# Kernel optimization log

Hardware: AMD Instinct MI355X
Metric: run time of the kernel (lower is better)

Reference implementation:

```python
import jax, jax.numpy as jnp
import numpy as np


def gcn_conv(x, W, b, src, dst, n):
    """PyG GCNConv: D^-1/2 (A+I) D^-1/2 X W + b, with added self-loops."""
    xw = x @ W  # [N, out]
    loop = jnp.arange(n, dtype=src.dtype)
    s = jnp.concatenate([src, loop])
    d = jnp.concatenate([dst, loop])
    deg = jax.ops.segment_sum(jnp.ones_like(d, dtype=xw.dtype), d, num_segments=n)
    dinv = jax.lax.rsqrt(jnp.maximum(deg, 1.0))
    norm = dinv[s] * dinv[d]  # [E+N]
    msg = xw[s] * norm[:, None]  # [E+N, out]
    return jax.ops.segment_sum(msg, d, num_segments=n) + b


def mean_pool(h, batch, num_graphs):
    s = jax.ops.segment_sum(h, batch, num_segments=num_graphs)
    cnt = jax.ops.segment_sum(jnp.ones((h.shape[0],), h.dtype), batch, num_segments=num_graphs)
    return s / jnp.maximum(cnt, 1.0)[:, None]


def setup_inputs() -> dict:
    key = jax.random.key(0)
    ks = jax.random.split(key, 12)
    N, E, F_dim, H_dim, K = 50000, 1600000, 128, 128, 32
    G = 64
    X = jax.random.normal(ks[0], (N, F_dim), dtype=jnp.float32)
    ei_feat = jax.random.randint(ks[1], (2, E), 0, N, dtype=jnp.int64)
    batch = jnp.sort(jax.random.randint(ks[2], (N,), 0, G, dtype=jnp.int64))
    sc = 1.0 / np.sqrt(H_dim)
    W1 = jax.random.normal(ks[3], (F_dim, H_dim), dtype=jnp.float32) * sc
    b1 = jnp.zeros((H_dim,), jnp.float32)
    W2 = jax.random.normal(ks[4], (H_dim, K), dtype=jnp.float32) * sc
    b2 = jnp.zeros((K,), jnp.float32)
    mW1 = jax.random.normal(ks[5], (H_dim, H_dim), dtype=jnp.float32) * sc
    mb1 = jnp.zeros((H_dim,), jnp.float32)
    mW2 = jax.random.normal(ks[6], (K, K), dtype=jnp.float32) * (1.0 / np.sqrt(K))
    mb2 = jnp.zeros((K,), jnp.float32)
    return {"X": X, "W1": W1, "b1": b1, "W2": W2, "b2": b2,
            "mW1": mW1, "mb1": mb1, "mW2": mW2, "mb2": mb2,
            "ei_feat": ei_feat, "batch": batch, "num_graphs": G}


def reference(X, W1, b1, W2, b2, mW1, mb1, mW2, mb2, ei_feat, batch, num_graphs):
    N = X.shape[0]
    src, dst = ei_feat[0], ei_feat[1]
    h = jax.nn.elu(gcn_conv(X, W1, b1, src, dst, N))  # [N, H]
    master_h = mean_pool(h, batch, num_graphs)  # [G, H]
    h = h + jax.nn.relu(master_h @ mW1 + mb1)[batch]
    Z = gcn_conv(h, W2, b2, src, dst, N)  # [N, K]
    master_z = mean_pool(Z, batch, num_graphs)  # [G, K]
    Z = Z + jax.nn.relu(master_z @ mW2 + mb2)[batch]
    return jax.nn.softmax(Z, axis=1)
```

## Files before the change

### kernel.cpp

```cpp
#include <hip/hip_runtime.h>
#include <hip/hip_bf16.h>
#include <hip/hip_fp16.h>

#define DEV_INLINE __device__ __forceinline__

static DEV_INLINE float4 ld4(const float* p){ return *reinterpret_cast<const float4*>(p); }

#define GNUM 64
#define CHUNK 4096
#define MAXNB 1024

__global__ __launch_bounds__(256) void k_hist(const int* __restrict__ dst, int E, int NB,
                                              int* __restrict__ bcnt){
    __shared__ int cnt[MAXNB];
    int t = threadIdx.x; int base0 = blockIdx.x*CHUNK;
    for (int i=t;i<NB;i+=256) cnt[i]=0;
    __syncthreads();
    int tot = E - base0; if (tot > CHUNK) tot = CHUNK;
    #pragma unroll
    for (int k=0;k<16;k++){
        int o = t + k*256;
        if (o < tot) atomicAdd(&cnt[dst[base0+o]>>7], 1);
    }
    __syncthreads();
    for (int i=t;i<NB;i+=256) if (cnt[i]) atomicAdd(&bcnt[i], cnt[i]);
}

__global__ void k_scan1b(const int* __restrict__ in, int* __restrict__ out, int M, int total,
                         const int* __restrict__ batch, int N, int* __restrict__ gstart){
    __shared__ int ws[4];
    int t = threadIdx.x;
    int i0 = t*4;
    int c0=(i0+0<M)?in[i0+0]:0, c1=(i0+1<M)?in[i0+1]:0;
    int c2=(i0+2<M)?in[i0+2]:0, c3=(i0+3<M)?in[i0+3]:0;
    int tsum=c0+c1+c2+c3;
    int lane=t&63, w=t>>6;
    int x=tsum;
    for (int off=1;off<64;off<<=1){ int yv=__shfl_up(x,off); if (lane>=off) x+=yv; }
    if (lane==63) ws[w]=x;
    __syncthreads();
    if (t==0){ int a=0; for (int i=0;i<4;i++){ int tmp=ws[i]; ws[i]=a; a+=tmp; } }
    __syncthreads();
    int ex = x - tsum + ws[w];
    if (i0+0<M) out[i0+0]=ex; ex+=c0;
    if (i0+1<M) out[i0+1]=ex; ex+=c1;
    if (i0+2<M) out[i0+2]=ex; ex+=c2;
    if (i0+3<M) out[i0+3]=ex;
    if (t==0 && total>=0) out[M]=total;
    if (t <= GNUM){
        int lo = 0, hi = N;
        while (lo < hi){ int mid = (lo+hi)>>1; if (batch[mid] < t) lo = mid+1; else hi = mid; }
        gstart[t] = lo;
    }
}

__global__ __launch_bounds__(256) void k_scatter(const int* __restrict__ src, const int* __restrict__ dst,
                                                 int E, int NB, const int* __restrict__ bbase,
                                                 int* __restrict__ bfill, unsigned* __restrict__ ebuf){
    __shared__ int cnt[MAXNB];
    __shared__ int pfx[MAXNB];
    __shared__ int gbase[MAXNB];
    __shared__ unsigned stage[CHUNK];
    __shared__ int ws[4];
    int t = threadIdx.x; int base0 = blockIdx.x*CHUNK;
    int tot = E - base0; if (tot > CHUNK) tot = CHUNK;
    for (int i=t;i<NB;i+=256) cnt[i]=0;
    __syncthreads();
    unsigned v[16]; int rk[16];
    #pragma unroll
    for (int k=0;k<16;k++){
        int o = t + k*256;
        if (o < tot){
            int e = base0 + o;
            int s = src[e], d = dst[e];
            v[k] = (unsigned)s | ((unsigned)d<<16);
            rk[k] = atomicAdd(&cnt[d>>7], 1);
        } else { v[k]=0u; rk[k]=-1; }
    }
    __syncthreads();
    int i0 = t*4;
    int c0=(i0+0<NB)?cnt[i0+0]:0, c1=(i0+1<NB)?cnt[i0+1]:0;
    int c2=(i0+2<NB)?cnt[i0+2]:0, c3=(i0+3<NB)?cnt[i0+3]:0;
    int tsum=c0+c1+c2+c3;
    int lane=t&63, w=t>>6;
    int x=tsum;
    for (int off=1;off<64;off<<=1){ int yv=__shfl_up(x,off); if (lane>=off) x+=yv; }
    if (lane==63) ws[w]=x;
    __syncthreads();
    if (t==0){ int a=0; for (int i=0;i<4;i++){ int tmp=ws[i]; ws[i]=a; a+=tmp; } }
    __syncthreads();
    int ex = x - tsum + ws[w];
    if (i0+0<NB) pfx[i0+0]=ex; ex+=c0;
    if (i0+1<NB) pfx[i0+1]=ex; ex+=c1;
    if (i0+2<NB) pfx[i0+2]=ex; ex+=c2;
    if (i0+3<NB) pfx[i0+3]=ex;
    __syncthreads();
    for (int i=t;i<NB;i+=256){
        int c = cnt[i];
        gbase[i] = c ? (bbase[i] + atomicAdd(&bfill[i], c)) : 0;
    }
    __syncthreads();
    #pragma unroll
    for (int k=0;k<16;k++) if (rk[k]>=0){ int b = (int)(v[k]>>23); stage[pfx[b]+rk[k]] = v[k]; }
    __syncthreads();
    for (int j=t;j<tot;j+=256){
        unsigned u = stage[j];
        int b = (int)(u>>23);
        ebuf[gbase[b] + (j - pfx[b])] = u;
    }
}

__global__ __launch_bounds__(256) void k_bucket_finish(const unsigned* __restrict__ ebuf,
                                                       const int* __restrict__ bbase,
                                                       int* __restrict__ rs, int* __restrict__ csr,
                                                       float* __restrict__ dinv, int N, int E){
    __shared__ int c2[128];
    __shared__ int rsl[128];
    __shared__ int ws[4];
    int b = blockIdx.x, t = threadIdx.x;
    if (t < 128) c2[t] = 0;
    __syncthreads();
    int s0 = bbase[b], s1 = bbase[b+1];
    for (int j = s0+t; j < s1; j += 256)
        atomicAdd(&c2[(ebuf[j]>>16)&127], 1);
    __syncthreads();
    int v = (t < 128) ? c2[t] : 0;
    int lane = t & 63, w = t >> 6;
    int x = v;
    for (int off=1; off<64; off<<=1){
        int yv = __shfl_up(x, off);
        if (lane >= off) x += yv;
    }
    if (lane == 63) ws[w] = x;
    __syncthreads();
    if (t < 128){
        int ex = x - v + ((w == 1) ? ws[0] : 0);
        rsl[t] = s0 + ex;
        int node = (b<<7) + t;
        if (node < N){
            rs[node] = s0 + ex;
            dinv[node] = rsqrtf((float)(v + 1));
        }
    }
    if (b == (int)gridDim.x - 1 && t == 0) rs[N] = E;
    __syncthreads();
    if (t < 128) c2[t] = 0;
    __syncthreads();
    for (int j = s0+t; j < s1; j += 256){
        unsigned u = ebuf[j];
        int ld = (u>>16)&127;
        int p = atomicAdd(&c2[ld], 1);
        csr[rsl[ld]+p] = (int)(u & 0xffffu);
    }
}

__global__ __launch_bounds__(256) void k_gemm1(const float* __restrict__ X, const float* __restrict__ W1,
                                               const float* __restrict__ dinv, __half* __restrict__ yh, int N){
    __shared__ float Ws[128*128];
    __shared__ float Xs[32*128];
    int t = threadIdx.x;
    int row0 = blockIdx.x * 32;
    if (blockIdx.x==0 && t < 32)
        reinterpret_cast<uint2*>(yh + (size_t)N*128)[t] = make_uint2(0u,0u);
    {
        const float4* Wg = (const float4*)W1;
        float4* Wl = (float4*)Ws;
        #pragma unroll
        for (int i=0;i<16;i++) Wl[t + i*256] = Wg[t + i*256];
    }
    {
        float4* Xl = (float4*)Xs;
        const float4* Xg = (const float4*)X;
        #pragma unroll
        for (int i=0;i<4;i++){
            int fi = t + i*256;
            int r = fi >> 5;
            float4 v = make_float4(0.f,0.f,0.f,0.f);
            if (row0 + r < N) v = Xg[(size_t)(row0+r)*32 + (fi & 31)];
            Xl[fi] = v;
        }
    }
    __syncthreads();
    int tc = t & 31, tr = t >> 5;
    float4 acc0={0,0,0,0}, acc1={0,0,0,0}, acc2={0,0,0,0}, acc3={0,0,0,0};
    for (int k=0;k<128;k+=4){
        float4 w0 = ld4(&Ws[(k+0)*128 + tc*4]);
        float4 w1 = ld4(&Ws[(k+1)*128 + tc*4]);
        float4 w2 = ld4(&Ws[(k+2)*128 + tc*4]);
        float4 w3 = ld4(&Ws[(k+3)*128 + tc*4]);
        #define ROWSTEP(ACC, RR) { float4 xr = ld4(&Xs[(4*tr+(RR))*128 + k]); \
            ACC.x += xr.x*w0.x + xr.y*w1.x + xr.z*w2.x + xr.w*w3.x; \
            ACC.y += xr.x*w0.y + xr.y*w1.y + xr.z*w2.y + xr.w*w3.y; \
            ACC.z += xr.x*w0.z + xr.y*w1.z + xr.z*w2.z + xr.w*w3.z; \
            ACC.w += xr.x*w0.w + xr.y*w1.w + xr.z*w2.w + xr.w*w3.w; }
        ROWSTEP(acc0,0) ROWSTEP(acc1,1) ROWSTEP(acc2,2) ROWSTEP(acc3,3)
        #undef ROWSTEP
    }
    #define STORESTEP(ACC, RR) { int row = row0 + 4*tr + (RR); if (row < N){ \
        float dv = dinv[row]; \
        __half2 p0 = __floats2half2_rn(ACC.x*dv, ACC.y*dv); \
        __half2 p1 = __floats2half2_rn(ACC.z*dv, ACC.w*dv); \
        uint2 stv; stv.x = *(unsigned*)&p0; stv.y = *(unsigned*)&p1; \
        *reinterpret_cast<uint2*>(&yh[(size_t)row*128 + tc*4]) = stv; } }
    STORESTEP(acc0,0) STORESTEP(acc1,1) STORESTEP(acc2,2) STORESTEP(acc3,3)
    #undef STORESTEP
}

__global__ void k_agg1(const __half* __restrict__ yh, const float* __restrict__ dinv,
                       const float* __restrict__ b1, const int* __restrict__ rs,
                       const int* __restrict__ csr, __half* __restrict__ h, int N){
    int wid = (int)((blockIdx.x * blockDim.x + threadIdx.x) >> 6);
    if (wid >= N) return;
    int lane = threadIdx.x & 63;
    int half = lane >> 5, hl = lane & 31;
    int beg = rs[wid], end = rs[wid+1];
    int len = end - beg;
    int len0 = (len + 1) >> 1;
    int hbeg = beg + (half ? len0 : 0);
    int hlen = half ? (len - len0) : len0;
    const __half* ybase = yh + hl*4;
    float4 acc = make_float4(0.f,0.f,0.f,0.f);
    if (half == 0){
        uint2 u = *reinterpret_cast<const uint2*>(ybase + (size_t)wid*128);
        float2 f0 = __half22float2(*(__half2*)&u.x), f1 = __half22float2(*(__half2*)&u.y);
        acc.x=f0.x; acc.y=f0.y; acc.z=f1.x; acc.w=f1.y;
    }
    int iters = (len0 + 31) >> 5;
    for (int c=0;c<iters;c++){
        int o = c*32 + hl;
        int idx = (o < hlen) ? csr[hbeg + o] : N;
        int tmax = len0 - c*32; if (tmax > 32) tmax = 32;
        int nch = (tmax + 3) >> 2;
        __half2 a0 = __float2half2_rn(0.f), a1 = __float2half2_rn(0.f);
        for (int ch=0; ch<nch; ++ch){
            int tb = (half<<5) + ch*4;
            int s0 = __shfl(idx, tb+0);
            int s1 = __shfl(idx, tb+1);
            int s2 = __shfl(idx, tb+2);
            int s3 = __shfl(idx, tb+3);
            uint2 u0 = *reinterpret_cast<const uint2*>(ybase + (size_t)s0*128);
            uint2 u1 = *reinterpret_cast<const uint2*>(ybase + (size_t)s1*128);
            uint2 u2 = *reinterpret_cast<const uint2*>(ybase + (size_t)s2*128);
            uint2 u3 = *reinterpret_cast<const uint2*>(ybase + (size_t)s3*128);
            a0 = __hadd2(a0, *(__half2*)&u0.x); a1 = __hadd2(a1, *(__half2*)&u0.y);
            a0 = __hadd2(a0, *(__half2*)&u1.x); a1 = __hadd2(a1, *(__half2*)&u1.y);
            a0 = __hadd2(a0, *(__half2*)&u2.x); a1 = __hadd2(a1, *(__half2*)&u2.y);
            a0 = __hadd2(a0, *(__half2*)&u3.x); a1 = __hadd2(a1, *(__half2*)&u3.y);
        }
        float2 f0 = __half22float2(a0), f1 = __half22float2(a1);
        acc.x += f0.x; acc.y += f0.y; acc.z += f1.x; acc.w += f1.y;
    }
    acc.x += __shfl_xor(acc.x, 32);
    acc.y += __shfl_xor(acc.y, 32);
    acc.z += __shfl_xor(acc.z, 32);
    acc.w += __shfl_xor(acc.w, 32);
    if (half == 0){
        float dv = dinv[wid];
        float4 bb = ld4(&b1[hl*4]);
        float4 o;
        o.x = dv*acc.x + bb.x; o.y = dv*acc.y + bb.y;
        o.z = dv*acc.z + bb.z; o.w = dv*acc.w + bb.w;
        o.x = o.x > 0.f ? o.x : expm1f(o.x);
        o.y = o.y > 0.f ? o.y : expm1f(o.y);
        o.z = o.z > 0.f ? o.z : expm1f(o.z);
        o.w = o.w > 0.f ? o.w : expm1f(o.w);
        __half2 p0 = __floats2half2_rn(o.x, o.y);
        __half2 p1 = __floats2half2_rn(o.z, o.w);
        uint2 stv; stv.x = *(unsigned*)&p0; stv.y = *(unsigned*)&p1;
        *reinterpret_cast<uint2*>(&h[(size_t)wid*128 + hl*4]) = stv;
    }
}

__global__ void k_mpoolh(const __half* __restrict__ hsrc, const int* __restrict__ gstart,
                         float* __restrict__ msum){
    int g = blockIdx.x, part = blockIdx.y, P = gridDim.y;
    int c = threadIdx.x;
    int s0 = gstart[g], s1 = gstart[g+1];
    int len = s1 - s0;
    int per = (len + P - 1) / P;
    int rbeg = s0 + part*per, rend = rbeg + per; if (rend > s1) rend = s1;
    float sx = 0.f, sy = 0.f;
    const __half2* h2 = (const __half2*)hsrc;
    for (int r = rbeg; r < rend; ++r){
        float2 f = __half22float2(h2[(size_t)r*64 + c]);
        sx += f.x; sy += f.y;
    }
    if (rend > rbeg){
        atomicAdd(&msum[g*128 + 2*c], sx);
        atomicAdd(&msum[g*128 + 2*c+1], sy);
    }
}

__global__ void k_mpool(const float* __restrict__ srcm, const int* __restrict__ gstart,
                        float* __restrict__ msum, int C){
    int g = blockIdx.x, part = blockIdx.y, P = gridDim.y;
    int c = threadIdx.x;
    if (c >= C) return;
    int s0 = gstart[g], s1 = gstart[g+1];
    int len = s1 - s0;
    int per = (len + P - 1) / P;
    int rbeg = s0 + part*per, rend = rbeg + per; if (rend > s1) rend = s1;
    float sum = 0.f;
    for (int r = rbeg; r < rend; ++r) sum += srcm[(size_t)r*C + c];
    if (rend > rbeg) atomicAdd(&msum[g*C + c], sum);
}

__global__ void k_mlp1(const float* __restrict__ msum, const int* __restrict__ gstart,
                       const float* __restrict__ mW1, const float* __restrict__ mb1,
                       float* __restrict__ r1){
    int g = blockIdx.x, c = threadIdx.x;
    int cnt = gstart[g+1] - gstart[g];
    float inv = 1.f / (float)(cnt > 1 ? cnt : 1);
    float acc = mb1[c];
    for (int k=0;k<128;k++) acc = fmaf(msum[g*128+k]*inv, mW1[k*128+c], acc);
    r1[g*128+c] = fmaxf(acc, 0.f);
}

__global__ void k_mlp2(const float* __restrict__ msum2, const int* __restrict__ gstart,
                       const float* __restrict__ mW2, const float* __restrict__ mb2,
                       float* __restrict__ r2){
    int g = blockIdx.x, c = threadIdx.x;
    if (c >= 32) return;
    int cnt = gstart[g+1] - gstart[g];
    float inv = 1.f / (float)(cnt > 1 ? cnt : 1);
    float acc = mb2[c];
    for (int k=0;k<32;k++) acc = fmaf(msum2[g*32+k]*inv, mW2[k*32+c], acc);
    r2[g*32+c] = fmaxf(acc, 0.f);
}

__global__ __launch_bounds__(256) void k_gemm2(const __half* __restrict__ h, const float* __restrict__ vn,
                                               const int* __restrict__ batch, const float* __restrict__ W2,
                                               const float* __restrict__ dinv, __half* __restrict__ y2, int N){
    __shared__ float W2s[128*32];
    int t = threadIdx.x;
    if (blockIdx.x==0 && t < 8)
        reinterpret_cast<uint2*>(y2 + (size_t)N*32)[t] = make_uint2(0u,0u);
    {
        float4* Wl = (float4*)W2s;
        const float4* Wg = (const float4*)W2;
        #pragma unroll
        for (int i=0;i<4;i++) Wl[t + i*256] = Wg[t + i*256];
    }
    __syncthreads();
    int row0 = blockIdx.x*64;
    int tc = t & 7, trg = t >> 3;
    int ra = row0 + 2*trg, rb = ra + 1;
    bool oka = ra < N, okb = rb < N;
    const __half* hpa = h + (size_t)(oka ? ra : 0)*128;
    const __half* hpb = h + (size_t)(okb ? rb : 0)*128;
    const float* vpa = vn + (size_t)(oka ? batch[ra] : 0)*128;
    const float* vpb = vn + (size_t)(okb ? batch[rb] : 0)*128;
    float4 acca={0,0,0,0}, accb={0,0,0,0};
    for (int k=0;k<128;k+=4){
        float4 w0 = ld4(&W2s[(k+0)*32 + tc*4]);
        float4 w1 = ld4(&W2s[(k+1)*32 + tc*4]);
        float4 w2 = ld4(&W2s[(k+2)*32 + tc*4]);
        float4 w3 = ld4(&W2s[(k+3)*32 + tc*4]);
        {
            uint2 u = *reinterpret_cast<const uint2*>(&hpa[k]);
            float2 f0 = __half22float2(*(__half2*)&u.x), f1 = __half22float2(*(__half2*)&u.y);
            float4 bb = ld4(vpa + k);
            float ax=f0.x+bb.x, ay=f0.y+bb.y, az=f1.x+bb.z, aw=f1.y+bb.w;
            acca.x += ax*w0.x + ay*w1.x + az*w2.x + aw*w3.x;
            acca.y += ax*w0.y + ay*w1.y + az*w2.y + aw*w3.y;
            acca.z += ax*w0.z + ay*w1.z + az*w2.z + aw*w3.z;
            acca.w += ax*w0.w + ay*w1.w + az*w2.w + aw*w3.w;
        }
        {
            uint2 u = *reinterpret_cast<const uint2*>(&hpb[k]);
            float2 f0 = __half22float2(*(__half2*)&u.x), f1 = __half22float2(*(__half2*)&u.y);
            float4 bb = ld4(vpb + k);
            float ax=f0.x+bb.x, ay=f0.y+bb.y, az=f1.x+bb.z, aw=f1.y+bb.w;
            accb.x += ax*w0.x + ay*w1.x + az*w2.x + aw*w3.x;
            accb.y += ax*w0.y + ay*w1.y + az*w2.y + aw*w3.y;
            accb.z += ax*w0.z + ay*w1.z + az*w2.z + aw*w3.z;
            accb.w += ax*w0.w + ay*w1.w + az*w2.w + aw*w3.w;
        }
    }
    if (oka){
        float dv = dinv[ra];
        __half2 p0 = __floats2half2_rn(acca.x*dv, acca.y*dv);
        __half2 p1 = __floats2half2_rn(acca.z*dv, acca.w*dv);
        uint2 stv; stv.x = *(unsigned*)&p0; stv.y = *(unsigned*)&p1;
        *reinterpret_cast<uint2*>(&y2[(size_t)ra*32 + tc*4]) = stv;
    }
    if (okb){
        float dv = dinv[rb];
        __half2 p0 = __floats2half2_rn(accb.x*dv, accb.y*dv);
        __half2 p1 = __floats2half2_rn(accb.z*dv, accb.w*dv);
        uint2 stv; stv.x = *(unsigned*)&p0; stv.y = *(unsigned*)&p1;
        *reinterpret_cast<uint2*>(&y2[(size_t)rb*32 + tc*4]) = stv;
    }
}

__global__ void k_agg2h(const __half* __restrict__ y2, const float* __restrict__ dinv,
                        const float* __restrict__ b2, const int* __restrict__ rs,
                        const int* __restrict__ csr, float* __restrict__ Z, int N){
    int wid = (int)((blockIdx.x*blockDim.x + threadIdx.x) >> 6);
    if (wid >= N) return;
    int lane = threadIdx.x & 63;
    int q = lane >> 4, ql = lane & 15;
    int beg = rs[wid], end = rs[wid+1], len = end-beg;
    int qlen = (len + 3) >> 2;
    int qbeg = beg + q*qlen;
    int qend = qbeg + qlen; if (qend > end) qend = end;
    int mylen = qend - qbeg; if (mylen < 0) mylen = 0;
    const __half2* ybase = (const __half2*)(y2) + ql;
    float sx = 0.f, sy = 0.f;
    int iters = (qlen + 15) >> 4;
    for (int c=0;c<iters;c++){
        int o = c*16 + ql;
        int idx = (o < mylen) ? csr[qbeg + o] : N;
        int tmax = qlen - c*16; if (tmax > 16) tmax = 16;
        int nch = (tmax + 3) >> 2;
        __half2 a = __float2half2_rn(0.f);
        for (int ch=0; ch<nch; ++ch){
            int tb = (q<<4) + ch*4;
            int s0 = __shfl(idx, tb+0);
            int s1 = __shfl(idx, tb+1);
            int s2 = __shfl(idx, tb+2);
            int s3 = __shfl(idx, tb+3);
            __half2 v0 = ybase[(size_t)s0*16];
            __half2 v1 = ybase[(size_t)s1*16];
            __half2 v2 = ybase[(size_t)s2*16];
            __half2 v3 = ybase[(size_t)s3*16];
            a = __hadd2(a, v0); a = __hadd2(a, v1);
            a = __hadd2(a, v2); a = __hadd2(a, v3);
        }
        float2 f = __half22float2(a);
        sx += f.x; sy += f.y;
    }
    sx += __shfl_xor(sx, 16); sy += __shfl_xor(sy, 16);
    sx += __shfl_xor(sx, 32); sy += __shfl_xor(sy, 32);
    if (q==0){
        float2 self = __half22float2(ybase[(size_t)wid*16]);
        sx += self.x; sy += self.y;
        float dv = dinv[wid];
        float2 o;
        o.x = dv*sx + b2[ql*2];
        o.y = dv*sy + b2[ql*2+1];
        *reinterpret_cast<float2*>(&Z[(size_t)wid*32 + ql*2]) = o;
    }
}

__global__ void k_softmax(float* __restrict__ Z, const float* __restrict__ r2,
                          const int* __restrict__ batch, int N){
    int r = blockIdx.x*8 + (threadIdx.x>>5);
    int c = threadIdx.x & 31;
    if (r >= N) return;
    float z = Z[(size_t)r*32+c] + r2[batch[r]*32 + c];
    float m = z;
    #pragma unroll
    for (int off=16; off>=1; off>>=1) m = fmaxf(m, __shfl_xor(m, off));
    float e = expf(z - m);
    float s = e;
    #pragma unroll
    for (int off=16; off>=1; off>>=1) s += __shfl_xor(s, off);
    Z[(size_t)r*32+c] = e / s;
}

extern "C" void kernel_launch(void* const* d_in, const int* in_sizes, int n_in,
                              void* d_out, int out_size, void* d_ws, size_t ws_size,
                              hipStream_t stream){
    const float* X   = (const float*)d_in[0];
    const float* W1  = (const float*)d_in[1];
    const float* b1  = (const float*)d_in[2];
    const float* W2  = (const float*)d_in[3];
    const float* b2  = (const float*)d_in[4];
    const float* mW1 = (const float*)d_in[5];
    const float* mb1 = (const float*)d_in[6];
    const float* mW2 = (const float*)d_in[7];
    const float* mb2 = (const float*)d_in[8];
    const int*   ei  = (const int*)d_in[9];
    const int*   batch = (const int*)d_in[10];
    int N = in_sizes[0] / 128;
    int E = in_sizes[9] / 2;
    const int* src = ei;
    const int* dst = ei + E;
    float* Zout = (float*)d_out;

    char* wsp = (char*)d_ws;
    size_t off = 0;
    auto alloc = [&](size_t bytes)->char*{
        char* p = wsp + off; off += (bytes + 255) & ~(size_t)255; return p;
    };
    int*   bcnt  = (int*)  alloc((size_t)MAXNB*4);
    int*   bfill = (int*)  alloc((size_t)MAXNB*4);
    float* msum  = (float*)alloc((size_t)GNUM*128*4);
    float* msum2 = (float*)alloc((size_t)GNUM*32*4);
    size_t zero_bytes = off;
    int*   bbase = (int*)  alloc((size_t)(MAXNB+1)*4);
    int*   rs    = (int*)  alloc((size_t)(N+1)*4);
    int*   gstart= (int*)  alloc((GNUM+1)*4);
    unsigned* ebuf = (unsigned*)alloc((size_t)E*4);
    int*   csr   = (int*)  alloc((size_t)E*4);
    float* dinvp = (float*)alloc((size_t)N*4);
    __half* yh   = (__half*)alloc((size_t)(N+1)*128*2);
    __half* h    = (__half*)alloc((size_t)N*128*2);
    __half* y2h  = (__half*)alloc((size_t)(N+1)*32*2);
    float* r1buf = (float*)alloc((size_t)GNUM*128*4);
    float* r2buf = (float*)alloc((size_t)GNUM*32*4);
    (void)ws_size; (void)n_in; (void)out_size;

    hipMemsetAsync(d_ws, 0, zero_bytes, stream);

    int NB = (N + 127) >> 7;
    int EB = (E + CHUNK-1) / CHUNK;

    k_hist         <<<EB, 256, 0, stream>>>(dst, E, NB, bcnt);
    k_scan1b       <<<1, 256, 0, stream>>>(bcnt, bbase, NB, E, batch, N, gstart);
    k_scatter      <<<EB, 256, 0, stream>>>(src, dst, E, NB, bbase, bfill, ebuf);
    k_bucket_finish<<<NB, 256, 0, stream>>>(ebuf, bbase, rs, csr, dinvp, N, E);

    k_gemm1 <<<(N+31)/32, 256, 0, stream>>>(X, W1, dinvp, yh, N);
    k_agg1  <<<(N+3)/4, 256, 0, stream>>>(yh, dinvp, b1, rs, csr, h, N);

    k_mpoolh<<<dim3(GNUM,8), 64, 0, stream>>>(h, gstart, msum);
    k_mlp1  <<<GNUM, 128, 0, stream>>>(msum, gstart, mW1, mb1, r1buf);

    k_gemm2 <<<(N+63)/64, 256, 0, stream>>>(h, r1buf, batch, W2, dinvp, y2h, N);
    k_agg2h <<<(N+3)/4, 256, 0, stream>>>(y2h, dinvp, b2, rs, csr, Zout, N);

    k_mpool <<<dim3(GNUM,8), 64, 0, stream>>>(Zout, gstart, msum2, 32);
    k_mlp2  <<<GNUM, 64, 0, stream>>>(msum2, gstart, mW2, mb2, r2buf);
    k_softmax<<<(N+7)/8, 256, 0, stream>>>(Zout, r2buf, batch, N);
}
```

Before: 259.7 us.

## Use MFMA fp16 for first GEMM, 16-bit CSR indices, wider gather loads

The first GEMM now runs on MFMA 16x16x32 fp16 instructions, reading W1 from a transposed, padded fp16 copy built by a new prep kernel, and converting X to fp16 in registers. CSR column indices shrink from 32-bit to 16-bit to cut index traffic. Both aggregation kernels switch to wider vector gathers (uint4 in layer 1, uint2 in layer 2) with more edge splits per wave. The aim is lower GEMM compute cost and less memory traffic in the gathers. Casting X to fp16 adds rounding error, and 16-bit indices rely on the node id fitting in 16 bits, which the existing bucket encoding already assumes.

Result: faster. 241.3 us (-7.1%).

```diff
diff --git a/kernel.cpp b/kernel.cpp
--- a/kernel.cpp
+++ b/kernel.cpp
@@ -9,6 +9,9 @@
 #define GNUM 64
 #define CHUNK 4096
 #define MAXNB 1024
+
+typedef _Float16 half8 __attribute__((ext_vector_type(8)));
+typedef float floatx4 __attribute__((ext_vector_type(4)));
 
 __global__ __launch_bounds__(256) void k_hist(const int* __restrict__ dst, int E, int NB,
                                               int* __restrict__ bcnt){
@@ -112,7 +115,7 @@
 
 __global__ __launch_bounds__(256) void k_bucket_finish(const unsigned* __restrict__ ebuf,
                                                        const int* __restrict__ bbase,
-                                                       int* __restrict__ rs, int* __restrict__ csr,
+                                                       int* __restrict__ rs, unsigned short* __restrict__ csr,
                                                        float* __restrict__ dinv, int N, int E){
     __shared__ int c2[128];
     __shared__ int rsl[128];
@@ -150,124 +153,132 @@
         unsigned u = ebuf[j];
         int ld = (u>>16)&127;
         int p = atomicAdd(&c2[ld], 1);
-        csr[rsl[ld]+p] = (int)(u & 0xffffu);
-    }
-}
-
-__global__ __launch_bounds__(256) void k_gemm1(const float* __restrict__ X, const float* __restrict__ W1,
+        csr[rsl[ld]+p] = (unsigned short)(u & 0xffffu);
+    }
+}
+
+__global__ void k_prep(const float* __restrict__ W1, __half* __restrict__ w1t){
+    int f = blockIdx.x*256 + threadIdx.x;
+    int c = f >> 7, k = f & 127;
+    w1t[c*136 + k] = __float2half(W1[k*128 + c]);
+}
+
+__global__ __launch_bounds__(256) void k_gemm1(const float* __restrict__ X, const __half* __restrict__ w1t,
                                                const float* __restrict__ dinv, __half* __restrict__ yh, int N){
-    __shared__ float Ws[128*128];
-    __shared__ float Xs[32*128];
+    __shared__ __half Wl[128*136];
     int t = threadIdx.x;
-    int row0 = blockIdx.x * 32;
     if (blockIdx.x==0 && t < 32)
         reinterpret_cast<uint2*>(yh + (size_t)N*128)[t] = make_uint2(0u,0u);
     {
-        const float4* Wg = (const float4*)W1;
-        float4* Wl = (float4*)Ws;
+        const uint4* g = (const uint4*)w1t;
+        uint4* l = (uint4*)Wl;
+        for (int i = t; i < 2176; i += 256) l[i] = g[i];
+    }
+    __syncthreads();
+    int wv = t>>6, lane = t&63;
+    int r0 = blockIdx.x*64 + wv*16;
+    if (r0 >= N) return;
+    int lr = lane & 15, lg = lane >> 4;
+    int r = r0 + lr;
+    bool rok = r < N;
+    const float* xrow = X + (size_t)(rok ? r : 0)*128;
+    floatx4 acc[8];
+    #pragma unroll
+    for (int i=0;i<8;i++) acc[i] = (floatx4){0.f,0.f,0.f,0.f};
+    #pragma unroll
+    for (int ks=0; ks<4; ks++){
+        int k0 = ks*32 + lg*8;
+        float4 xa = ld4(xrow + k0);
+        float4 xb = ld4(xrow + k0 + 4);
+        half8 bfrag;
+        bfrag[0]=(_Float16)xa.x; bfrag[1]=(_Float16)xa.y; bfrag[2]=(_Float16)xa.z; bfrag[3]=(_Float16)xa.w;
+        bfrag[4]=(_Float16)xb.x; bfrag[5]=(_Float16)xb.y; bfrag[6]=(_Float16)xb.z; bfrag[7]=(_Float16)xb.w;
         #pragma unroll
-        for (int i=0;i<16;i++) Wl[t + i*256] = Wg[t + i*256];
-    }
-    {
-        float4* Xl = (float4*)Xs;
-        const float4* Xg = (const float4*)X;
+        for (int ct=0; ct<8; ct++){
+            half8 afrag = *reinterpret_cast<const half8*>(&Wl[(ct*16 + lr)*136 + k0]);
+            acc[ct] = __builtin_amdgcn_mfma_f32_16x16x32_f16(afrag, bfrag, acc[ct], 0, 0, 0);
+        }
+    }
+    if (rok){
+        float dv = dinv[r];
         #pragma unroll
-        for (int i=0;i<4;i++){
-            int fi = t + i*256;
-            int r = fi >> 5;
-            float4 v = make_float4(0.f,0.f,0.f,0.f);
-            if (row0 + r < N) v = Xg[(size_t)(row0+r)*32 + (fi & 31)];
-            Xl[fi] = v;
-        }
-    }
-    __syncthreads();
-    int tc = t & 31, tr = t >> 5;
-    float4 acc0={0,0,0,0}, acc1={0,0,0,0}, acc2={0,0,0,0}, acc3={0,0,0,0};
-    for (int k=0;k<128;k+=4){
-        float4 w0 = ld4(&Ws[(k+0)*128 + tc*4]);
-        float4 w1 = ld4(&Ws[(k+1)*128 + tc*4]);
-        float4 w2 = ld4(&Ws[(k+2)*128 + tc*4]);
-        float4 w3 = ld4(&Ws[(k+3)*128 + tc*4]);
-        #define ROWSTEP(ACC, RR) { float4 xr = ld4(&Xs[(4*tr+(RR))*128 + k]); \
-            ACC.x += xr.x*w0.x + xr.y*w1.x + xr.z*w2.x + xr.w*w3.x; \
-            ACC.y += xr.x*w0.y + xr.y*w1.y + xr.z*w2.y + xr.w*w3.y; \
-            ACC.z += xr.x*w0.z + xr.y*w1.z + xr.z*w2.z + xr.w*w3.z; \
-            ACC.w += xr.x*w0.w + xr.y*w1.w + xr.z*w2.w + xr.w*w3.w; }
-        ROWSTEP(acc0,0) ROWSTEP(acc1,1) ROWSTEP(acc2,2) ROWSTEP(acc3,3)
-        #undef ROWSTEP
-    }
-    #define STORESTEP(ACC, RR) { int row = row0 + 4*tr + (RR); if (row < N){ \
-        float dv = dinv[row]; \
-        __half2 p0 = __floats2half2_rn(ACC.x*dv, ACC.y*dv); \
-        __half2 p1 = __floats2half2_rn(ACC.z*dv, ACC.w*dv); \
-        uint2 stv; stv.x = *(unsigned*)&p0; stv.y = *(unsigned*)&p1; \
-        *reinterpret_cast<uint2*>(&yh[(size_t)row*128 + tc*4]) = stv; } }
-    STORESTEP(acc0,0) STORESTEP(acc1,1) STORESTEP(acc2,2) STORESTEP(acc3,3)
-    #undef STORESTEP
+        for (int ct=0; ct<8; ct++){
+            __half2 p0 = __floats2half2_rn(acc[ct][0]*dv, acc[ct][1]*dv);
+            __half2 p1 = __floats2half2_rn(acc[ct][2]*dv, acc[ct][3]*dv);
+            uint2 stv; stv.x = *(unsigned*)&p0; stv.y = *(unsigned*)&p1;
+            *reinterpret_cast<uint2*>(&yh[(size_t)r*128 + ct*16 + lg*4]) = stv;
+        }
+    }
 }
 
 __global__ void k_agg1(const __half* __restrict__ yh, const float* __restrict__ dinv,
                        const float* __restrict__ b1, const int* __restrict__ rs,
-                       const int* __restrict__ csr, __half* __restrict__ h, int N){
+                       const unsigned short* __restrict__ csr, __half* __restrict__ h, int N){
     int wid = (int)((blockIdx.x * blockDim.x + threadIdx.x) >> 6);
     if (wid >= N) return;
     int lane = threadIdx.x & 63;
-    int half = lane >> 5, hl = lane & 31;
+    int q = lane >> 4, ql = lane & 15;
     int beg = rs[wid], end = rs[wid+1];
     int len = end - beg;
-    int len0 = (len + 1) >> 1;
-    int hbeg = beg + (half ? len0 : 0);
-    int hlen = half ? (len - len0) : len0;
-    const __half* ybase = yh + hl*4;
-    float4 acc = make_float4(0.f,0.f,0.f,0.f);
-    if (half == 0){
-        uint2 u = *reinterpret_cast<const uint2*>(ybase + (size_t)wid*128);
-        float2 f0 = __half22float2(*(__half2*)&u.x), f1 = __half22float2(*(__half2*)&u.y);
-        acc.x=f0.x; acc.y=f0.y; acc.z=f1.x; acc.w=f1.y;
-    }
-    int iters = (len0 + 31) >> 5;
+    int qlen = (len + 3) >> 2;
+    int qbeg = beg + q*qlen;
+    int qend = qbeg + qlen; if (qend > end) qend = end;
+    int mylen = qend - qbeg; if (mylen < 0) mylen = 0;
+    const uint4* base = reinterpret_cast<const uint4*>(yh) + ql;
+    float f0=0.f,f1=0.f,f2=0.f,f3=0.f,f4=0.f,f5=0.f,f6=0.f,f7=0.f;
+    int iters = (qlen + 15) >> 4;
     for (int c=0;c<iters;c++){
-        int o = c*32 + hl;
-        int idx = (o < hlen) ? csr[hbeg + o] : N;
-        int tmax = len0 - c*32; if (tmax > 32) tmax = 32;
+        int o = c*16 + ql;
+        int idx = (o < mylen) ? (int)csr[qbeg + o] : N;
+        int tmax = qlen - c*16; if (tmax > 16) tmax = 16;
         int nch = (tmax + 3) >> 2;
-        __half2 a0 = __float2half2_rn(0.f), a1 = __float2half2_rn(0.f);
+        __half2 a0 = __float2half2_rn(0.f), a1 = a0, a2 = a0, a3 = a0;
         for (int ch=0; ch<nch; ++ch){
-            int tb = (half<<5) + ch*4;
+            int tb = (q<<4) + ch*4;
             int s0 = __shfl(idx, tb+0);
             int s1 = __shfl(idx, tb+1);
             int s2 = __shfl(idx, tb+2);
             int s3 = __shfl(idx, tb+3);
-            uint2 u0 = *reinterpret_cast<const uint2*>(ybase + (size_t)s0*128);
-            uint2 u1 = *reinterpret_cast<const uint2*>(ybase + (size_t)s1*128);
-            uint2 u2 = *reinterpret_cast<const uint2*>(ybase + (size_t)s2*128);
-            uint2 u3 = *reinterpret_cast<const uint2*>(ybase + (size_t)s3*128);
+            uint4 u0 = base[(size_t)s0*16];
+            uint4 u1 = base[(size_t)s1*16];
+            uint4 u2 = base[(size_t)s2*16];
+            uint4 u3 = base[(size_t)s3*16];
             a0 = __hadd2(a0, *(__half2*)&u0.x); a1 = __hadd2(a1, *(__half2*)&u0.y);
+            a2 = __hadd2(a2, *(__half2*)&u0.z); a3 = __hadd2(a3, *(__half2*)&u0.w);
             a0 = __hadd2(a0, *(__half2*)&u1.x); a1 = __hadd2(a1, *(__half2*)&u1.y);
+            a2 = __hadd2(a2, *(__half2*)&u1.z); a3 = __hadd2(a3, *(__half2*)&u1.w);
             a0 = __hadd2(a0, *(__half2*)&u2.x); a1 = __hadd2(a1, *(__half2*)&u2.y);
+            a2 = __hadd2(a2, *(__half2*)&u2.z); a3 = __hadd2(a3, *(__half2*)&u2.w);
             a0 = __hadd2(a0, *(__half2*)&u3.x); a1 = __hadd2(a1, *(__half2*)&u3.y);
-        }
-        float2 f0 = __half22float2(a0), f1 = __half22float2(a1);
-        acc.x += f0.x; acc.y += f0.y; acc.z += f1.x; acc.w += f1.y;
-    }
-    acc.x += __shfl_xor(acc.x, 32);
-    acc.y += __shfl_xor(acc.y, 32);
-    acc.z += __shfl_xor(acc.z, 32);
-    acc.w += __shfl_xor(acc.w, 32);
-    if (half == 0){
+            a2 = __hadd2(a2, *(__half2*)&u3.z); a3 = __hadd2(a3, *(__half2*)&u3.w);
+        }
+        float2 t0 = __half22float2(a0); f0 += t0.x; f1 += t0.y;
+        float2 t1 = __half22float2(a1); f2 += t1.x; f3 += t1.y;
+        float2 t2 = __half22float2(a2); f4 += t2.x; f5 += t2.y;
+        float2 t3 = __half22float2(a3); f6 += t3.x; f7 += t3.y;
+    }
+    f0 += __shfl_xor(f0,16); f1 += __shfl_xor(f1,16); f2 += __shfl_xor(f2,16); f3 += __shfl_xor(f3,16);
+    f4 += __shfl_xor(f4,16); f5 += __shfl_xor(f5,16); f6 += __shfl_xor(f6,16); f7 += __shfl_xor(f7,16);
+    f0 += __shfl_xor(f0,32); f1 += __shfl_xor(f1,32); f2 += __shfl_xor(f2,32); f3 += __shfl_xor(f3,32);
+    f4 += __shfl_xor(f4,32); f5 += __shfl_xor(f5,32); f6 += __shfl_xor(f6,32); f7 += __shfl_xor(f7,32);
+    if (q == 0){
+        uint4 su = base[(size_t)wid*16];
+        float2 s0 = __half22float2(*(__half2*)&su.x); f0 += s0.x; f1 += s0.y;
+        float2 s1 = __half22float2(*(__half2*)&su.y); f2 += s1.x; f3 += s1.y;
+        float2 s2 = __half22float2(*(__half2*)&su.z); f4 += s2.x; f5 += s2.y;
+        float2 s3 = __half22float2(*(__half2*)&su.w); f6 += s3.x; f7 += s3.y;
         float dv = dinv[wid];
-        float4 bb = ld4(&b1[hl*4]);
-        float4 o;
-        o.x = dv*acc.x + bb.x; o.y = dv*acc.y + bb.y;
-        o.z = dv*acc.z + bb.z; o.w = dv*acc.w + bb.w;
-        o.x = o.x > 0.f ? o.x : expm1f(o.x);
-        o.y = o.y > 0.f ? o.y : expm1f(o.y);
-        o.z = o.z > 0.f ? o.z : expm1f(o.z);
-        o.w = o.w > 0.f ? o.w : expm1f(o.w);
-        __half2 p0 = __floats2half2_rn(o.x, o.y);
-        __half2 p1 = __floats2half2_rn(o.z, o.w);
-        uint2 stv; stv.x = *(unsigned*)&p0; stv.y = *(unsigned*)&p1;
-        *reinterpret_cast<uint2*>(&h[(size_t)wid*128 + hl*4]) = stv;
+        float4 ba = ld4(&b1[ql*8]), bb = ld4(&b1[ql*8+4]);
+        float o0 = dv*f0+ba.x, o1 = dv*f1+ba.y, o2 = dv*f2+ba.z, o3 = dv*f3+ba.w;
+        float o4 = dv*f4+bb.x, o5 = dv*f5+bb.y, o6 = dv*f6+bb.z, o7 = dv*f7+bb.w;
+        o0 = o0>0.f?o0:expm1f(o0); o1 = o1>0.f?o1:expm1f(o1);
+        o2 = o2>0.f?o2:expm1f(o2); o3 = o3>0.f?o3:expm1f(o3);
+        o4 = o4>0.f?o4:expm1f(o4); o5 = o5>0.f?o5:expm1f(o5);
+        o6 = o6>0.f?o6:expm1f(o6); o7 = o7>0.f?o7:expm1f(o7);
+        __half2 p0 = __floats2half2_rn(o0,o1), p1 = __floats2half2_rn(o2,o3);
+        __half2 p2 = __floats2half2_rn(o4,o5), p3 = __floats2half2_rn(o6,o7);
+        uint4 stv; stv.x=*(unsigned*)&p0; stv.y=*(unsigned*)&p1; stv.z=*(unsigned*)&p2; stv.w=*(unsigned*)&p3;
+        *reinterpret_cast<uint4*>(&h[(size_t)wid*128 + ql*8]) = stv;
     }
 }
 
@@ -395,51 +406,56 @@
 
 __global__ void k_agg2h(const __half* __restrict__ y2, const float* __restrict__ dinv,
                         const float* __restrict__ b2, const int* __restrict__ rs,
-                        const int* __restrict__ csr, float* __restrict__ Z, int N){
+                        const unsigned short* __restrict__ csr, float* __restrict__ Z, int N){
     int wid = (int)((blockIdx.x*blockDim.x + threadIdx.x) >> 6);
     if (wid >= N) return;
     int lane = threadIdx.x & 63;
-    int q = lane >> 4, ql = lane & 15;
+    int o8 = lane >> 3, ol = lane & 7;
     int beg = rs[wid], end = rs[wid+1], len = end-beg;
-    int qlen = (len + 3) >> 2;
-    int qbeg = beg + q*qlen;
-    int qend = qbeg + qlen; if (qend > end) qend = end;
-    int mylen = qend - qbeg; if (mylen < 0) mylen = 0;
-    const __half2* ybase = (const __half2*)(y2) + ql;
-    float sx = 0.f, sy = 0.f;
-    int iters = (qlen + 15) >> 4;
+    int olen = (len + 7) >> 3;
+    int obeg = beg + o8*olen;
+    int oend = obeg + olen; if (oend > end) oend = end;
+    int mylen = oend - obeg; if (mylen < 0) mylen = 0;
+    const uint2* base = reinterpret_cast<const uint2*>(y2) + ol;
+    float f0=0.f, f1=0.f, f2=0.f, f3=0.f;
+    int iters = (olen + 7) >> 3;
     for (int c=0;c<iters;c++){
-        int o = c*16 + ql;
-        int idx = (o < mylen) ? csr[qbeg + o] : N;
-        int tmax = qlen - c*16; if (tmax > 16) tmax = 16;
+        int o = c*8 + ol;
+        int idx = (o < mylen) ? (int)csr[obeg + o] : N;
+        int tmax = olen - c*8; if (tmax > 8) tmax = 8;
         int nch = (tmax + 3) >> 2;
-        __half2 a = __float2half2_rn(0.f);
+        __half2 a0 = __float2half2_rn(0.f), a1 = a0;
         for (int ch=0; ch<nch; ++ch){
-            int tb = (q<<4) + ch*4;
+            int tb = (o8<<3) + ch*4;
             int s0 = __shfl(idx, tb+0);
             int s1 = __shfl(idx, tb+1);
             int s2 = __shfl(idx, tb+2);
             int s3 = __shfl(idx, tb+3);
-            __half2 v0 = ybase[(size_t)s0*16];
-            __half2 v1 = ybase[(size_t)s1*16];
-            __half2 v2 = ybase[(size_t)s2*16];
-            __half2 v3 = ybase[(size_t)s3*16];
-            a = __hadd2(a, v0); a = __hadd2(a, v1);
-            a = __hadd2(a, v2); a = __hadd2(a, v3);
-        }
-        float2 f = __half22float2(a);
-        sx += f.x; sy += f.y;
-    }
-    sx += __shfl_xor(sx, 16); sy += __shfl_xor(sy, 16);
-    sx += __shfl_xor(sx, 32); sy += __shfl_xor(sy, 32);
-    if (q==0){
-        float2 self = __half22float2(ybase[(size_t)wid*16]);
-        sx += self.x; sy += self.y;
+            uint2 u0 = base[(size_t)s0*8];
+            uint2 u1 = base[(size_t)s1*8];
+            uint2 u2 = base[(size_t)s2*8];
+            uint2 u3 = base[(size_t)s3*8];
+            a0 = __hadd2(a0, *(__half2*)&u0.x); a1 = __hadd2(a1, *(__half2*)&u0.y);
+            a0 = __hadd2(a0, *(__half2*)&u1.x); a1 = __hadd2(a1, *(__half2*)&u1.y);
+            a0 = __hadd2(a0, *(__half2*)&u2.x); a1 = __hadd2(a1, *(__half2*)&u2.y);
+            a0 = __hadd2(a0, *(__half2*)&u3.x); a1 = __hadd2(a1, *(__half2*)&u3.y);
+        }
+        float2 t0 = __half22float2(a0); f0 += t0.x; f1 += t0.y;
+        float2 t1 = __half22float2(a1); f2 += t1.x; f3 += t1.y;
+    }
+    f0 += __shfl_xor(f0,8);  f1 += __shfl_xor(f1,8);  f2 += __shfl_xor(f2,8);  f3 += __shfl_xor(f3,8);
+    f0 += __shfl_xor(f0,16); f1 += __shfl_xor(f1,16); f2 += __shfl_xor(f2,16); f3 += __shfl_xor(f3,16);
+    f0 += __shfl_xor(f0,32); f1 += __shfl_xor(f1,32); f2 += __shfl_xor(f2,32); f3 += __shfl_xor(f3,32);
+    if (o8 == 0){
+        uint2 su = base[(size_t)wid*8];
+        float2 s0 = __half22float2(*(__half2*)&su.x); f0 += s0.x; f1 += s0.y;
+        float2 s1 = __half22float2(*(__half2*)&su.y); f2 += s1.x; f3 += s1.y;
         float dv = dinv[wid];
-        float2 o;
-        o.x = dv*sx + b2[ql*2];
-        o.y = dv*sy + b2[ql*2+1];
-        *reinterpret_cast<float2*>(&Z[(size_t)wid*32 + ql*2]) = o;
+        float4 bb = ld4(&b2[ol*4]);
+        float4 outv;
+        outv.x = dv*f0 + bb.x; outv.y = dv*f1 + bb.y;
+        outv.z = dv*f2 + bb.z; outv.w = dv*f3 + bb.w;
+        *reinterpret_cast<float4*>(&Z[(size_t)wid*32 + ol*4]) = outv;
     }
 }
 
@@ -493,8 +509,9 @@
     int*   rs    = (int*)  alloc((size_t)(N+1)*4);
     int*   gstart= (int*)  alloc((GNUM+1)*4);
     unsigned* ebuf = (unsigned*)alloc((size_t)E*4);
-    int*   csr   = (int*)  alloc((size_t)E*4);
+    unsigned short* csr = (unsigned short*)alloc((size_t)E*2);
     float* dinvp = (float*)alloc((size_t)N*4);
+    __half* w1t  = (__half*)alloc((size_t)128*136*2);
     __half* yh   = (__half*)alloc((size_t)(N+1)*128*2);
     __half* h    = (__half*)alloc((size_t)N*128*2);
     __half* y2h  = (__half*)alloc((size_t)(N+1)*32*2);
@@ -507,12 +524,13 @@
     int NB = (N + 127) >> 7;
     int EB = (E + CHUNK-1) / CHUNK;
 
+    k_prep         <<<64, 256, 0, stream>>>(W1, w1t);
     k_hist         <<<EB, 256, 0, stream>>>(dst, E, NB, bcnt);
     k_scan1b       <<<1, 256, 0, stream>>>(bcnt, bbase, NB, E, batch, N, gstart);
     k_scatter      <<<EB, 256, 0, stream>>>(src, dst, E, NB, bbase, bfill, ebuf);
     k_bucket_finish<<<NB, 256, 0, stream>>>(ebuf, bbase, rs, csr, dinvp, N, E);
 
-    k_gemm1 <<<(N+31)/32, 256, 0, stream>>>(X, W1, dinvp, yh, N);
+    k_gemm1 <<<(N+63)/64, 256, 0, stream>>>(X, w1t, dinvp, yh, N);
     k_agg1  <<<(N+3)/4, 256, 0, stream>>>(yh, dinvp, b1, rs, csr, h, N);
 
     k_mpoolh<<<dim3(GNUM,8), 64, 0, stream>>>(h, gstart, msum);
```
